# Kernel optimization log

Measured on AMD Instinct MI355X. Metric: run time of the kernel, lower is better.

The kernel has to match this reference:

```python
import jax, jax.numpy as jnp
import numpy as np

H = 8        # num_heads
D = 64       # qkv_dim
E = 512      # embed_dim = H*D
MS = 16      # ms_hidden_dim


def setup_inputs() -> dict:
    key = jax.random.key(0)
    ks = jax.random.split(key, 12)
    b, r, c = 4, 512, 512
    row_emb = jax.random.normal(ks[0], (b, r, E), dtype=jnp.float32)
    col_emb = jax.random.normal(ks[1], (b, c, E), dtype=jnp.float32)
    cost_mat = jax.random.uniform(ks[2], (b, r, c), dtype=jnp.float32)
    attn_mask = jax.random.randint(ks[3], (b, H, r, c), 0, 2) > 0
    s = 1.0 / np.sqrt(E)
    Wq = jax.random.uniform(ks[4], (H * D, E), minval=-s, maxval=s)
    Wk = jax.random.uniform(ks[5], (H * D, E), minval=-s, maxval=s)
    Wv = jax.random.uniform(ks[6], (H * D, E), minval=-s, maxval=s)
    Wout = jax.random.uniform(ks[7], (E, E), minval=-s, maxval=s)
    m1 = np.sqrt(0.5)
    m2 = np.sqrt(1.0 / MS)
    Wmix1 = jax.random.uniform(ks[8], (H * MS, 2 * H), minval=-m1, maxval=m1)
    Wmix2 = jax.random.uniform(ks[9], (H, H * MS), minval=-m2, maxval=m2)
    return {"row_emb": row_emb, "col_emb": col_emb, "cost_mat": cost_mat,
            "attn_mask": attn_mask, "Wq": Wq, "Wk": Wk, "Wv": Wv,
            "Wmix1": Wmix1, "Wmix2": Wmix2, "Wout": Wout}


def reference(row_emb, col_emb, cost_mat, attn_mask, Wq, Wk, Wv, Wmix1, Wmix2, Wout):
    b, r, _ = row_emb.shape
    c = col_emb.shape[1]
    norm = 1.0 / jnp.sqrt(jnp.asarray(D, row_emb.dtype))
    # projections -> [b, h, s, d]
    q = (row_emb @ Wq.T).reshape(b, r, H, D).transpose(0, 2, 1, 3)
    k = (col_emb @ Wk.T).reshape(b, c, H, D).transpose(0, 2, 1, 3)
    v = (col_emb @ Wv.T).reshape(b, c, H, D).transpose(0, 2, 1, 3)
    dot = norm * jnp.einsum('bhrd,bhcd->bhrc', q, k)            # [b,h,r,c]
    cost = jnp.broadcast_to(cost_mat[:, None, :, :], dot.shape)  # [b,h,r,c]
    # stack then rearrange 'b h r c s -> b r c (h s)' (h major, s minor)
    two = jnp.stack([dot, cost], axis=-1)                        # [b,h,r,c,2]
    two = two.transpose(0, 2, 3, 1, 4).reshape(b, r, c, 2 * H)
    hid = jax.nn.relu(two @ Wmix1.T)                             # [b,r,c,H*MS]
    ms = hid @ Wmix2.T                                           # [b,r,c,H]
    logits = ms.transpose(0, 3, 1, 2)                            # [b,h,r,c]
    # mask handling: rows that are fully masked become fully unmasked
    all_masked = jnp.all(attn_mask, axis=-1, keepdims=True)
    mask = jnp.where(all_masked, False, attn_mask)
    logits = jnp.where(mask, -jnp.inf, logits)
    weights = jax.nn.softmax(logits, axis=-1)
    out = jnp.einsum('bhrc,bhcd->bhrd', weights, v)              # [b,h,r,d]
    out = out.transpose(0, 2, 1, 3).reshape(b, r, H * D)         # b s (h d)
    return out @ Wout.T
```

## Files before the change

### kernel.cpp

```cpp
#include <hip/hip_runtime.h>
#include <math.h>

typedef __attribute__((ext_vector_type(8))) short bf16x8;
typedef __attribute__((ext_vector_type(4))) float f32x4;
typedef unsigned short ushort_t;

static __device__ inline unsigned short f2bf(float f) {
    union { float f; unsigned u; } v; v.f = f;
    unsigned r = v.u + 0x7fff + ((v.u >> 16) & 1);
    return (unsigned short)(r >> 16);
}

#if defined(__has_builtin)
#  if __has_builtin(__builtin_amdgcn_cvt_pk_bf16_f32)
#    define HAVE_PK_BF16 1
#  endif
#endif

static __device__ inline unsigned pk2bf(float a, float b) {
#ifdef HAVE_PK_BF16
    auto r = __builtin_amdgcn_cvt_pk_bf16_f32(a, b);
    unsigned u; __builtin_memcpy(&u, &r, 4);
    return u;
#else
    return (unsigned)f2bf(a) | ((unsigned)f2bf(b) << 16);
#endif
}

__global__ __launch_bounds__(256) void convert_all(const float* __restrict__ a0,
                                                   const float* __restrict__ a1,
                                                   const float* __restrict__ a2,
                                                   const float* __restrict__ a3,
                                                   const float* __restrict__ a4,
                                                   const float* __restrict__ a5,
                                                   ushort_t* __restrict__ dst) {
    const size_t e = ((size_t)blockIdx.x * 256 + threadIdx.x) * 4;
    const float* src; size_t off;
    if      (e < 1048576) { src = a0; off = 0; }
    else if (e < 2097152) { src = a1; off = 1048576; }
    else if (e < 2359296) { src = a2; off = 2097152; }
    else if (e < 2621440) { src = a3; off = 2359296; }
    else if (e < 2883584) { src = a4; off = 2621440; }
    else                  { src = a5; off = 2883584; }
    const float4 v = *(const float4*)(src + (e - off));
    uint2 o; o.x = pk2bf(v.x, v.y); o.y = pk2bf(v.z, v.w);
    *(uint2*)(dst + e) = o;
}

__global__ __launch_bounds__(256) void gemm_qkv(const ushort_t* __restrict__ rowb,
                                                const ushort_t* __restrict__ colb,
                                                const ushort_t* __restrict__ Wqb,
                                                const ushort_t* __restrict__ Wkb,
                                                const ushort_t* __restrict__ Wvb,
                                                ushort_t* __restrict__ Qb,
                                                ushort_t* __restrict__ Kb,
                                                ushort_t* __restrict__ Vt) {
    const int z = blockIdx.z;
    const ushort_t* A = (z == 0) ? rowb : colb;
    const ushort_t* B = (z == 0) ? Wqb : (z == 1) ? Wkb : Wvb;

    const int t    = threadIdx.x;
    const int w    = t >> 6;
    const int lane = t & 63;
    const int quad = lane >> 4;
    const int sl   = lane & 15;
    const int m0 = blockIdx.x * 64 + (w >> 1) * 32;
    const int n0 = blockIdx.y * 64 + (w & 1) * 32;

    const ushort_t* ap0 = A + (size_t)(m0 + sl) * 512 + quad * 8;
    const ushort_t* ap1 = A + (size_t)(m0 + 16 + sl) * 512 + quad * 8;
    const ushort_t* bp0 = B + (size_t)(n0 + sl) * 512 + quad * 8;
    const ushort_t* bp1 = B + (size_t)(n0 + 16 + sl) * 512 + quad * 8;

    f32x4 acc[2][2] = {};

    bf16x8 a0 = *(const bf16x8*)ap0;
    bf16x8 a1 = *(const bf16x8*)ap1;
    bf16x8 b0 = *(const bf16x8*)bp0;
    bf16x8 b1 = *(const bf16x8*)bp1;

    for (int ks = 0; ks < 16; ++ks) {
        bf16x8 na0, na1, nb0, nb1;
        if (ks < 15) {
            const int k0 = (ks + 1) * 32;
            na0 = *(const bf16x8*)(ap0 + k0);
            na1 = *(const bf16x8*)(ap1 + k0);
            nb0 = *(const bf16x8*)(bp0 + k0);
            nb1 = *(const bf16x8*)(bp1 + k0);
        }
        acc[0][0] = __builtin_amdgcn_mfma_f32_16x16x32_bf16(a0, b0, acc[0][0], 0, 0, 0);
        acc[0][1] = __builtin_amdgcn_mfma_f32_16x16x32_bf16(a0, b1, acc[0][1], 0, 0, 0);
        acc[1][0] = __builtin_amdgcn_mfma_f32_16x16x32_bf16(a1, b0, acc[1][0], 0, 0, 0);
        acc[1][1] = __builtin_amdgcn_mfma_f32_16x16x32_bf16(a1, b1, acc[1][1], 0, 0, 0);
        a0 = na0; a1 = na1; b0 = nb0; b1 = nb1;
    }

#pragma unroll
    for (int rs = 0; rs < 2; ++rs)
#pragma unroll
        for (int cs = 0; cs < 2; ++cs) {
            const int n = n0 + cs * 16 + sl;
            if (z == 2) {
                const int mb   = m0 + rs * 16 + quad * 4;
                const int bidx = mb >> 9, c = mb & 511;
                const int h = n >> 6, d = n & 63;
                ushort4 o;
                o.x = f2bf(acc[rs][cs][0]); o.y = f2bf(acc[rs][cs][1]);
                o.z = f2bf(acc[rs][cs][2]); o.w = f2bf(acc[rs][cs][3]);
                *(ushort4*)(Vt + (size_t)(((bidx * 8 + h) * 64 + d)) * 512 + c) = o;
            } else {
                ushort_t* C = (z == 0) ? Qb : Kb;
#pragma unroll
                for (int reg = 0; reg < 4; ++reg) {
                    const int m = m0 + rs * 16 + quad * 4 + reg;
                    C[(size_t)m * 512 + n] = f2bf(acc[rs][cs][reg]);
                }
            }
        }
}

__global__ __launch_bounds__(256) void gemm_out(const ushort_t* __restrict__ A,
                                                const ushort_t* __restrict__ B,
                                                float* __restrict__ C) {
    const int t    = threadIdx.x;
    const int w    = t >> 6;
    const int lane = t & 63;
    const int quad = lane >> 4;
    const int sl   = lane & 15;
    const int m0 = blockIdx.x * 64 + (w >> 1) * 32;
    const int n0 = blockIdx.y * 64 + (w & 1) * 32;

    const ushort_t* ap0 = A + (size_t)(m0 + sl) * 512 + quad * 8;
    const ushort_t* ap1 = A + (size_t)(m0 + 16 + sl) * 512 + quad * 8;
    const ushort_t* bp0 = B + (size_t)(n0 + sl) * 512 + quad * 8;
    const ushort_t* bp1 = B + (size_t)(n0 + 16 + sl) * 512 + quad * 8;

    f32x4 acc[2][2] = {};

    bf16x8 a0 = *(const bf16x8*)ap0;
    bf16x8 a1 = *(const bf16x8*)ap1;
    bf16x8 b0 = *(const bf16x8*)bp0;
    bf16x8 b1 = *(const bf16x8*)bp1;

    for (int ks = 0; ks < 16; ++ks) {
        bf16x8 na0, na1, nb0, nb1;
        if (ks < 15) {
            const int k0 = (ks + 1) * 32;
            na0 = *(const bf16x8*)(ap0 + k0);
            na1 = *(const bf16x8*)(ap1 + k0);
            nb0 = *(const bf16x8*)(bp0 + k0);
            nb1 = *(const bf16x8*)(bp1 + k0);
        }
        acc[0][0] = __builtin_amdgcn_mfma_f32_16x16x32_bf16(a0, b0, acc[0][0], 0, 0, 0);
        acc[0][1] = __builtin_amdgcn_mfma_f32_16x16x32_bf16(a0, b1, acc[0][1], 0, 0, 0);
        acc[1][0] = __builtin_amdgcn_mfma_f32_16x16x32_bf16(a1, b0, acc[1][0], 0, 0, 0);
        acc[1][1] = __builtin_amdgcn_mfma_f32_16x16x32_bf16(a1, b1, acc[1][1], 0, 0, 0);
        a0 = na0; a1 = na1; b0 = nb0; b1 = nb1;
    }

#pragma unroll
    for (int rs = 0; rs < 2; ++rs)
#pragma unroll
        for (int cs = 0; cs < 2; ++cs) {
            const int n = n0 + cs * 16 + sl;
#pragma unroll
            for (int reg = 0; reg < 4; ++reg) {
                const int m = m0 + rs * 16 + quad * 4 + reg;
                C[(size_t)m * 512 + n] = acc[rs][cs][reg];
            }
        }
}

__global__ __launch_bounds__(512) void dot_mlp_v5(const ushort_t* __restrict__ Qb,
                                                  const ushort_t* __restrict__ Kb,
                                                  const float* __restrict__ cost,
                                                  const float* __restrict__ W1,
                                                  const float* __restrict__ W2,
                                                  float* __restrict__ logits) {
    __shared__ ushort_t Xs[1024 * 18];
    __shared__ ushort_t hidS[8 * 16 * 36];
    __shared__ ushort_t W1fs[128 * 16];
    __shared__ ushort_t W2ss[8 * 128];

    const int b  = blockIdx.z;
    const int r0 = blockIdx.y * 32;
    const int c0 = blockIdx.x * 32;
    const int t    = threadIdx.x;
    const int w    = t >> 6;
    const int lane = t & 63;
    const int quad = lane >> 4;
    const int sl   = lane & 15;

    const bf16x8 zf = {0, 0, 0, 0, 0, 0, 0, 0};

    if (t < 128) {
        float s = 0.f;
#pragma unroll
        for (int h = 0; h < 8; ++h) {
            W1fs[t * 16 + h] = f2bf(W1[t * 16 + 2 * h]);
            s += W1[t * 16 + 2 * h + 1];
        }
        W1fs[t * 16 + 8] = f2bf(s);
#pragma unroll
        for (int k = 9; k < 16; ++k) W1fs[t * 16 + k] = 0;
    }
#pragma unroll
    for (int i = 0; i < 2; ++i) W2ss[t + i * 512] = f2bf(W2[t + i * 512]);

#pragma unroll
    for (int i = 0; i < 2; ++i) {
        const int cell = t + i * 512;
        const int rl = cell >> 5, cl = cell & 31;
        unsigned* base = (unsigned*)(Xs + cell * 18 + 8);
        base[0] = (unsigned)f2bf(cost[((size_t)b * 512 + r0 + rl) * 512 + c0 + cl]);
        base[1] = 0; base[2] = 0; base[3] = 0; base[4] = 0;
    }

    {
        const int hp = w & 3;
        const int h0 = hp * 2;
        const int rs = w >> 2;
        bf16x8 af[2][2], bfr[2][2][2];
#pragma unroll
        for (int hh = 0; hh < 2; ++hh)
#pragma unroll
            for (int ks = 0; ks < 2; ++ks) {
                af[hh][ks] = *(const bf16x8*)(Qb +
                    ((size_t)(b * 512 + r0 + rs * 16 + sl) * 512 + (h0 + hh) * 64 + ks * 32 + quad * 8));
#pragma unroll
                for (int cs = 0; cs < 2; ++cs)
                    bfr[hh][cs][ks] = *(const bf16x8*)(Kb +
                        ((size_t)(b * 512 + c0 + cs * 16 + sl) * 512 + (h0 + hh) * 64 + ks * 32 + quad * 8));
            }
        f32x4 dacc[2][2];
#pragma unroll
        for (int hh = 0; hh < 2; ++hh)
#pragma unroll
            for (int cs = 0; cs < 2; ++cs) {
                f32x4 acc = {0.f, 0.f, 0.f, 0.f};
                acc = __builtin_amdgcn_mfma_f32_16x16x32_bf16(af[hh][0], bfr[hh][cs][0], acc, 0, 0, 0);
                acc = __builtin_amdgcn_mfma_f32_16x16x32_bf16(af[hh][1], bfr[hh][cs][1], acc, 0, 0, 0);
                dacc[hh][cs] = acc;
            }
#pragma unroll
        for (int cs = 0; cs < 2; ++cs)
#pragma unroll
            for (int reg = 0; reg < 4; ++reg) {
                const int cell = (rs * 16 + quad * 4 + reg) * 32 + cs * 16 + sl;
                ((unsigned*)Xs)[cell * 9 + hp] =
                    pk2bf(dacc[0][cs][reg] * 0.125f, dacc[1][cs][reg] * 0.125f);
            }
    }

    __syncthreads();

    bf16x8 bw1[8];
#pragma unroll
    for (int nt = 0; nt < 8; ++nt)
        bw1[nt] = (quad < 2) ? *(const bf16x8*)&W1fs[(nt * 16 + sl) * 16 + quad * 8] : zf;
    bf16x8 bw2[4];
#pragma unroll
    for (int ks = 0; ks < 4; ++ks) {
        union { ushort_t s[8]; bf16x8 v; } tu;
#pragma unroll
        for (int i = 0; i < 8; ++i) {
            const int p  = quad * 8 + i;
            const int jc = (p >> 1) | ((p & 1) << 4);
            tu.s[i] = (sl < 8) ? W2ss[sl * 128 + ks * 32 + jc] : (ushort_t)0;
        }
        bw2[ks] = tu.v;
    }

    ushort_t* hidW = hidS + w * (16 * 36);

#pragma unroll
    for (int mt = 0; mt < 8; ++mt) {
        const int gmt = w * 8 + mt;
        const int cb  = gmt * 16;

        bf16x8 a1 = zf;
        if (quad < 2) {
            const unsigned* xr = (const unsigned*)Xs + (size_t)(cb + sl) * 9 + quad * 4;
            union { unsigned u[4]; bf16x8 v; } tmp;
            tmp.u[0] = xr[0]; tmp.u[1] = xr[1]; tmp.u[2] = xr[2]; tmp.u[3] = xr[3];
            a1 = tmp.v;
        }

        f32x4 acc2 = {0.f, 0.f, 0.f, 0.f};
#pragma unroll
        for (int ks = 0; ks < 4; ++ks) {
            f32x4 z = {0.f, 0.f, 0.f, 0.f};
            const f32x4 h0 = __builtin_amdgcn_mfma_f32_16x16x32_bf16(a1, bw1[2 * ks],     z, 0, 0, 0);
            const f32x4 h1 = __builtin_amdgcn_mfma_f32_16x16x32_bf16(a1, bw1[2 * ks + 1], z, 0, 0, 0);
#pragma unroll
            for (int rp = 0; rp < 4; ++rp)
                ((unsigned*)hidW)[(quad * 4 + rp) * 18 + sl] =
                    pk2bf(fmaxf(h0[rp], 0.f), fmaxf(h1[rp], 0.f));
            union { uint2 u2[2]; bf16x8 v; } tu;
            const ushort_t* hp2 = hidW + sl * 36 + quad * 8;
            tu.u2[0] = *(const uint2*)hp2;
            tu.u2[1] = *(const uint2*)(hp2 + 4);
            acc2 = __builtin_amdgcn_mfma_f32_16x16x32_bf16(tu.v, bw2[ks], acc2, 0, 0, 0);
        }

        if (sl < 8) {
            const int r = r0 + (gmt >> 1);
            const int cbase = c0 + (gmt & 1) * 16 + quad * 4;
            float4 o; o.x = acc2[0]; o.y = acc2[1]; o.z = acc2[2]; o.w = acc2[3];
            *(float4*)&logits[((size_t)(b * 8 + sl) * 512 + r) * 512 + cbase] = o;
        }
    }
}

__global__ __launch_bounds__(256) void softmax_pv(const float* __restrict__ logits,
                                                  const int* __restrict__ mask,
                                                  const ushort_t* __restrict__ Vt,
                                                  ushort_t* __restrict__ Aout) {
    __shared__ ushort_t Ps[16 * 520];

    const int t    = threadIdx.x;
    const int w    = t >> 6;
    const int lane = t & 63;
    const int quad = lane >> 4;
    const int sl   = lane & 15;
    const int rt = blockIdx.x;
    const int bh = blockIdx.y;
    const int r0 = rt * 16;

#pragma unroll
    for (int rr = 0; rr < 4; ++rr) {
        const int row = w * 4 + rr;
        const float* lp = logits + ((size_t)bh * 512 + r0 + row) * 512;
        const int*   mp = mask   + ((size_t)bh * 512 + r0 + row) * 512;

        float v[8]; int m[8]; int allm = 1;
#pragma unroll
        for (int i = 0; i < 8; ++i) {
            v[i] = lp[lane + i * 64];
            m[i] = mp[lane + i * 64];
            allm &= (m[i] != 0);
        }
        const bool all_masked = (__all(allm) != 0);

        float mx = -__builtin_inff();
#pragma unroll
        for (int i = 0; i < 8; ++i) {
            const bool keep = all_masked || (m[i] == 0);
            if (keep) mx = fmaxf(mx, v[i]);
        }
#pragma unroll
        for (int s = 32; s > 0; s >>= 1) mx = fmaxf(mx, __shfl_xor(mx, s, 64));

        float e[8]; float sum = 0.f;
#pragma unroll
        for (int i = 0; i < 8; ++i) {
            const bool keep = all_masked || (m[i] == 0);
            e[i] = keep ? __expf(v[i] - mx) : 0.f;
            sum += e[i];
        }
#pragma unroll
        for (int s = 32; s > 0; s >>= 1) sum += __shfl_xor(sum, s, 64);

        const float inv = 1.f / sum;
#pragma unroll
        for (int i = 0; i < 8; ++i)
            Ps[row * 520 + lane + i * 64] = f2bf(e[i] * inv);
    }

    __syncthreads();

    const int n0w = w * 16;
    const ushort_t* vb = Vt + (size_t)bh * 64 * 512;

    f32x4 acc = {0.f, 0.f, 0.f, 0.f};
    for (int ks = 0; ks < 16; ++ks) {
        union { uint2 u2[2]; bf16x8 v; } ta;
        const ushort_t* pp = Ps + (size_t)sl * 520 + ks * 32 + quad * 8;
        ta.u2[0] = *(const uint2*)pp;
        ta.u2[1] = *(const uint2*)(pp + 4);
        const bf16x8 bv = *(const bf16x8*)(vb + (size_t)(n0w + sl) * 512 + ks * 32 + quad * 8);
        acc = __builtin_amdgcn_mfma_f32_16x16x32_bf16(ta.v, bv, acc, 0, 0, 0);
    }

    const int bidx = bh >> 3, h = bh & 7;
    ushort_t* Cb = Aout + (size_t)bidx * 512 * 512 + h * 64;
    const int n = n0w + sl;
#pragma unroll
    for (int reg = 0; reg < 4; ++reg) {
        const int m = r0 + quad * 4 + reg;
        Cb[(size_t)m * 512 + n] = f2bf(acc[reg]);
    }
}

extern "C" void kernel_launch(void* const* d_in, const int* in_sizes, int n_in,
                              void* d_out, int out_size, void* d_ws, size_t ws_size,
                              hipStream_t stream) {
    const float* row_emb = (const float*)d_in[0];
    const float* col_emb = (const float*)d_in[1];
    const float* cost    = (const float*)d_in[2];
    const int*   mask    = (const int*)d_in[3];
    const float* Wq      = (const float*)d_in[4];
    const float* Wk      = (const float*)d_in[5];
    const float* Wv      = (const float*)d_in[6];
    const float* Wmix1   = (const float*)d_in[7];
    const float* Wmix2   = (const float*)d_in[8];
    const float* Wout    = (const float*)d_in[9];
    float* out = (float*)d_out;

    char* ws = (char*)d_ws;
    const size_t MB = (size_t)1 << 20;
    ushort_t* convDst = (ushort_t*)ws;
    ushort_t* rowb  = (ushort_t*)(ws);
    ushort_t* colb  = (ushort_t*)(ws + 2 * MB);
    ushort_t* Wqb   = (ushort_t*)(ws + 4 * MB);
    ushort_t* Wkb   = (ushort_t*)(ws + 4 * MB + 512 * 1024);
    ushort_t* Wvb   = (ushort_t*)(ws + 5 * MB);
    ushort_t* Woutb = (ushort_t*)(ws + 5 * MB + 512 * 1024);
    ushort_t* Qb    = (ushort_t*)(ws + 6 * MB);
    ushort_t* Kb    = (ushort_t*)(ws + 8 * MB);
    ushort_t* Vt    = (ushort_t*)(ws + 10 * MB);
    ushort_t* Aoutb = (ushort_t*)(ws + 12 * MB);
    float* logitsBuf = (float*)(ws + 16 * MB);

    convert_all<<<3072, 256, 0, stream>>>(row_emb, col_emb, Wq, Wk, Wv, Wout, convDst);

    gemm_qkv<<<dim3(32, 8, 3), 256, 0, stream>>>(rowb, colb, Wqb, Wkb, Wvb, Qb, Kb, Vt);

    dot_mlp_v5<<<dim3(16, 16, 4), 512, 0, stream>>>(Qb, Kb, cost, Wmix1, Wmix2, logitsBuf);

    softmax_pv<<<dim3(32, 32), 256, 0, stream>>>(logitsBuf, mask, Vt, Aoutb);

    gemm_out<<<dim3(32, 8), 256, 0, stream>>>(Aoutb, Woutb, out);
}
```

Measured before the change: 190.6 us.

## Fuse masked exp into MLP logits kernel and defer softmax normalization

The mixing-MLP kernel now applies the mask and exponentiates the logits directly, writing unnormalized bf16 probabilities and per-block partial row sums. The all-masked-row flags are precomputed by extra blocks appended to the conversion kernel. The PV kernel no longer runs a softmax pass; it reads the bf16 probabilities from global memory and divides by the summed partials at output. This halves the intermediate traffic (bf16 instead of fp32) and drops a full softmax pass. The price is skipping the max subtraction, which risks overflow for large logits.

```diff
diff --git a/kernel.cpp b/kernel.cpp
--- a/kernel.cpp
+++ b/kernel.cpp
@@ -27,24 +27,40 @@
 #endif
 }
 
-__global__ __launch_bounds__(256) void convert_all(const float* __restrict__ a0,
-                                                   const float* __restrict__ a1,
-                                                   const float* __restrict__ a2,
-                                                   const float* __restrict__ a3,
-                                                   const float* __restrict__ a4,
-                                                   const float* __restrict__ a5,
-                                                   ushort_t* __restrict__ dst) {
-    const size_t e = ((size_t)blockIdx.x * 256 + threadIdx.x) * 4;
-    const float* src; size_t off;
-    if      (e < 1048576) { src = a0; off = 0; }
-    else if (e < 2097152) { src = a1; off = 1048576; }
-    else if (e < 2359296) { src = a2; off = 2097152; }
-    else if (e < 2621440) { src = a3; off = 2359296; }
-    else if (e < 2883584) { src = a4; off = 2621440; }
-    else                  { src = a5; off = 2883584; }
-    const float4 v = *(const float4*)(src + (e - off));
-    uint2 o; o.x = pk2bf(v.x, v.y); o.y = pk2bf(v.z, v.w);
-    *(uint2*)(dst + e) = o;
+__global__ __launch_bounds__(256) void convert_allm(const float* __restrict__ a0,
+                                                    const float* __restrict__ a1,
+                                                    const float* __restrict__ a2,
+                                                    const float* __restrict__ a3,
+                                                    const float* __restrict__ a4,
+                                                    const float* __restrict__ a5,
+                                                    const int* __restrict__ mask,
+                                                    ushort_t* __restrict__ dst,
+                                                    int* __restrict__ allmOut) {
+    if (blockIdx.x < 3072) {
+        const size_t e = ((size_t)blockIdx.x * 256 + threadIdx.x) * 4;
+        const float* src; size_t off;
+        if      (e < 1048576) { src = a0; off = 0; }
+        else if (e < 2097152) { src = a1; off = 1048576; }
+        else if (e < 2359296) { src = a2; off = 2097152; }
+        else if (e < 2621440) { src = a3; off = 2359296; }
+        else if (e < 2883584) { src = a4; off = 2621440; }
+        else                  { src = a5; off = 2883584; }
+        const float4 v = *(const float4*)(src + (e - off));
+        uint2 o; o.x = pk2bf(v.x, v.y); o.y = pk2bf(v.z, v.w);
+        *(uint2*)(dst + e) = o;
+    } else {
+        const int bid  = blockIdx.x - 3072;
+        const int w    = threadIdx.x >> 6;
+        const int lane = threadIdx.x & 63;
+        const int row  = bid * 4 + w;
+        const int* mp = mask + (size_t)row * 512 + lane * 8;
+        const int4 m0 = *(const int4*)mp;
+        const int4 m1 = *(const int4*)(mp + 4);
+        const int allv = (m0.x && m0.y && m0.z && m0.w &&
+                          m1.x && m1.y && m1.z && m1.w);
+        const int res = (__all(allv) != 0) ? 1 : 0;
+        if (lane == 0) allmOut[row] = res;
+    }
 }
 
 __global__ __launch_bounds__(256) void gemm_qkv(const ushort_t* __restrict__ rowb,
@@ -171,12 +187,15 @@
         }
 }
 
-__global__ __launch_bounds__(512) void dot_mlp_v5(const ushort_t* __restrict__ Qb,
+__global__ __launch_bounds__(512) void dot_mlp_v7(const ushort_t* __restrict__ Qb,
                                                   const ushort_t* __restrict__ Kb,
                                                   const float* __restrict__ cost,
                                                   const float* __restrict__ W1,
                                                   const float* __restrict__ W2,
-                                                  float* __restrict__ logits) {
+                                                  const int* __restrict__ mask,
+                                                  const int* __restrict__ allm,
+                                                  ushort_t* __restrict__ tbuf,
+                                                  float* __restrict__ lpart) {
     __shared__ ushort_t Xs[1024 * 18];
     __shared__ ushort_t hidS[8 * 16 * 36];
     __shared__ ushort_t W1fs[128 * 16];
@@ -273,6 +292,8 @@
 
     ushort_t* hidW = hidS + w * (16 * 36);
 
+    float rsum[4] = {0.f, 0.f, 0.f, 0.f};
+
 #pragma unroll
     for (int mt = 0; mt < 8; ++mt) {
         const int gmt = w * 8 + mt;
@@ -303,20 +324,41 @@
             acc2 = __builtin_amdgcn_mfma_f32_16x16x32_bf16(tu.v, bw2[ks], acc2, 0, 0, 0);
         }
 
+        float psum = 0.f;
         if (sl < 8) {
             const int r = r0 + (gmt >> 1);
             const int cbase = c0 + (gmt & 1) * 16 + quad * 4;
-            float4 o; o.x = acc2[0]; o.y = acc2[1]; o.z = acc2[2]; o.w = acc2[3];
-            *(float4*)&logits[((size_t)(b * 8 + sl) * 512 + r) * 512 + cbase] = o;
-        }
-    }
-}
-
-__global__ __launch_bounds__(256) void softmax_pv(const float* __restrict__ logits,
-                                                  const int* __restrict__ mask,
-                                                  const ushort_t* __restrict__ Vt,
-                                                  ushort_t* __restrict__ Aout) {
-    __shared__ ushort_t Ps[16 * 520];
+            const size_t rowoff = (size_t)(b * 8 + sl) * 512 + r;
+            const int4 m4 = *(const int4*)(mask + rowoff * 512 + cbase);
+            const int av = allm[rowoff];
+            float tv0 = (av || !m4.x) ? __expf(acc2[0]) : 0.f;
+            float tv1 = (av || !m4.y) ? __expf(acc2[1]) : 0.f;
+            float tv2 = (av || !m4.z) ? __expf(acc2[2]) : 0.f;
+            float tv3 = (av || !m4.w) ? __expf(acc2[3]) : 0.f;
+            ushort4 o;
+            o.x = f2bf(tv0); o.y = f2bf(tv1); o.z = f2bf(tv2); o.w = f2bf(tv3);
+            *(ushort4*)&tbuf[rowoff * 512 + cbase] = o;
+            psum = tv0 + tv1 + tv2 + tv3;
+        }
+        psum += __shfl_xor(psum, 16, 64);
+        psum += __shfl_xor(psum, 32, 64);
+        rsum[mt >> 1] += psum;
+    }
+
+    if (quad == 0 && sl < 8) {
+#pragma unroll
+        for (int i = 0; i < 4; ++i) {
+            const size_t rowoff = (size_t)(b * 8 + sl) * 512 + (r0 + w * 4 + i);
+            lpart[rowoff * 16 + blockIdx.x] = rsum[i];
+        }
+    }
+}
+
+__global__ __launch_bounds__(256) void pv_norm(const ushort_t* __restrict__ tbuf,
+                                               const float* __restrict__ lpart,
+                                               const ushort_t* __restrict__ Vt,
+                                               ushort_t* __restrict__ Aout) {
+    __shared__ float lsum[16];
 
     const int t    = threadIdx.x;
     const int w    = t >> 6;
@@ -327,59 +369,26 @@
     const int bh = blockIdx.y;
     const int r0 = rt * 16;
 
-#pragma unroll
-    for (int rr = 0; rr < 4; ++rr) {
-        const int row = w * 4 + rr;
-        const float* lp = logits + ((size_t)bh * 512 + r0 + row) * 512;
-        const int*   mp = mask   + ((size_t)bh * 512 + r0 + row) * 512;
-
-        float v[8]; int m[8]; int allm = 1;
-#pragma unroll
-        for (int i = 0; i < 8; ++i) {
-            v[i] = lp[lane + i * 64];
-            m[i] = mp[lane + i * 64];
-            allm &= (m[i] != 0);
-        }
-        const bool all_masked = (__all(allm) != 0);
-
-        float mx = -__builtin_inff();
-#pragma unroll
-        for (int i = 0; i < 8; ++i) {
-            const bool keep = all_masked || (m[i] == 0);
-            if (keep) mx = fmaxf(mx, v[i]);
-        }
-#pragma unroll
-        for (int s = 32; s > 0; s >>= 1) mx = fmaxf(mx, __shfl_xor(mx, s, 64));
-
-        float e[8]; float sum = 0.f;
-#pragma unroll
-        for (int i = 0; i < 8; ++i) {
-            const bool keep = all_masked || (m[i] == 0);
-            e[i] = keep ? __expf(v[i] - mx) : 0.f;
-            sum += e[i];
-        }
-#pragma unroll
-        for (int s = 32; s > 0; s >>= 1) sum += __shfl_xor(sum, s, 64);
-
-        const float inv = 1.f / sum;
-#pragma unroll
-        for (int i = 0; i < 8; ++i)
-            Ps[row * 520 + lane + i * 64] = f2bf(e[i] * inv);
-    }
-
+    if (t < 16) {
+        const float* lp = lpart + ((size_t)bh * 512 + r0 + t) * 16;
+        const float4 s0 = *(const float4*)lp;
+        const float4 s1 = *(const float4*)(lp + 4);
+        const float4 s2 = *(const float4*)(lp + 8);
+        const float4 s3 = *(const float4*)(lp + 12);
+        lsum[t] = (s0.x + s0.y + s0.z + s0.w) + (s1.x + s1.y + s1.z + s1.w) +
+                  (s2.x + s2.y + s2.z + s2.w) + (s3.x + s3.y + s3.z + s3.w);
+    }
     __syncthreads();
 
+    const ushort_t* tb = tbuf + (size_t)bh * 512 * 512;
+    const ushort_t* vb = Vt + (size_t)bh * 64 * 512;
     const int n0w = w * 16;
-    const ushort_t* vb = Vt + (size_t)bh * 64 * 512;
 
     f32x4 acc = {0.f, 0.f, 0.f, 0.f};
     for (int ks = 0; ks < 16; ++ks) {
-        union { uint2 u2[2]; bf16x8 v; } ta;
-        const ushort_t* pp = Ps + (size_t)sl * 520 + ks * 32 + quad * 8;
-        ta.u2[0] = *(const uint2*)pp;
-        ta.u2[1] = *(const uint2*)(pp + 4);
+        const bf16x8 ta = *(const bf16x8*)(tb + (size_t)(r0 + sl) * 512 + ks * 32 + quad * 8);
         const bf16x8 bv = *(const bf16x8*)(vb + (size_t)(n0w + sl) * 512 + ks * 32 + quad * 8);
-        acc = __builtin_amdgcn_mfma_f32_16x16x32_bf16(ta.v, bv, acc, 0, 0, 0);
+        acc = __builtin_amdgcn_mfma_f32_16x16x32_bf16(ta, bv, acc, 0, 0, 0);
     }
 
     const int bidx = bh >> 3, h = bh & 7;
@@ -388,7 +397,8 @@
 #pragma unroll
     for (int reg = 0; reg < 4; ++reg) {
         const int m = r0 + quad * 4 + reg;
-        Cb[(size_t)m * 512 + n] = f2bf(acc[reg]);
+        const float inv = 1.f / lsum[quad * 4 + reg];
+        Cb[(size_t)m * 512 + n] = f2bf(acc[reg] * inv);
     }
 }
 
@@ -420,15 +430,19 @@
     ushort_t* Kb    = (ushort_t*)(ws + 8 * MB);
     ushort_t* Vt    = (ushort_t*)(ws + 10 * MB);
     ushort_t* Aoutb = (ushort_t*)(ws + 12 * MB);
-    float* logitsBuf = (float*)(ws + 16 * MB);
-
-    convert_all<<<3072, 256, 0, stream>>>(row_emb, col_emb, Wq, Wk, Wv, Wout, convDst);
+    ushort_t* tbuf  = (ushort_t*)(ws + 16 * MB);
+    float* lpart    = (float*)(ws + 34 * MB);
+    int* allmBuf    = (int*)(ws + 35 * MB);
+
+    convert_allm<<<7168, 256, 0, stream>>>(row_emb, col_emb, Wq, Wk, Wv, Wout,
+                                           mask, convDst, allmBuf);
 
     gemm_qkv<<<dim3(32, 8, 3), 256, 0, stream>>>(rowb, colb, Wqb, Wkb, Wvb, Qb, Kb, Vt);
 
-    dot_mlp_v5<<<dim3(16, 16, 4), 512, 0, stream>>>(Qb, Kb, cost, Wmix1, Wmix2, logitsBuf);
-
-    softmax_pv<<<dim3(32, 32), 256, 0, stream>>>(logitsBuf, mask, Vt, Aoutb);
+    dot_mlp_v7<<<dim3(16, 16, 4), 512, 0, stream>>>(Qb, Kb, cost, Wmix1, Wmix2,
+                                                    mask, allmBuf, tbuf, lpart);
+
+    pv_norm<<<dim3(32, 32), 256, 0, stream>>>(tbuf, lpart, Vt, Aoutb);
 
     gemm_out<<<dim3(32, 8), 256, 0, stream>>>(Aoutb, Woutb, out);
 }
```

New measurement: 193.2 us. No clear change (+1.4%).
